# Performance work log

Measured on AMD Instinct MI355X. Metric: run time of the kernel, lower is better.

The kernel has to match this reference:

```python
import jax, jax.numpy as jnp
import numpy as np

N = 50000
E = 800000
DIM = 256
H = 8
HD = DIM // H


def setup_inputs() -> dict:
    key = jax.random.key(0)
    ks = jax.random.split(key, 8)
    s = 0.02
    return {
        "x": jax.random.normal(ks[0], (N, DIM), jnp.float32),
        "src": jax.random.randint(ks[1], (E,), 0, N, jnp.int32),
        "dst": jax.random.randint(ks[2], (E,), 0, N, jnp.int32),
        "Wqkv": jax.random.normal(ks[3], (DIM, 3 * DIM), jnp.float32) * s,
        "bqkv": jnp.zeros((3 * DIM,), jnp.float32),
        "Wout": jax.random.normal(ks[4], (DIM, DIM), jnp.float32) * s,
        "bout": jnp.zeros((DIM,), jnp.float32),
        "W1": jax.random.normal(ks[5], (2 * DIM, DIM), jnpp := jnp.float32) * s,
        "b1": jnp.zeros((DIM,), jnp.float32),
        "W2": jax.random.normal(ks[6], (DIM, DIM), jnp.float32) * s,
        "b2": jnp.zeros((DIM,), jnp.float32),
    }


def reference(x, src, dst, Wqkv, bqkv, Wout, bout, W1, b1, W2, b2):
    n = x.shape[0]
    scale = 1.0 / np.sqrt(HD).astype(np.float32)
    # QKV projection; torch reshapes [N, 3*dim] -> [N, H, 3*hd] then splits per head
    qkv = (x @ Wqkv + bqkv).reshape(n, H, 3 * HD)
    q, k, v = qkv[..., :HD], qkv[..., HD:2 * HD], qkv[..., 2 * HD:]
    # per-edge attention scores: key at src dotted with query at dst -> [E, H]
    scores = jnp.einsum('ehd,ehd->eh', k[src], q[dst]) * scale
    # edge softmax grouped by destination node
    m = jax.ops.segment_max(scores, dst, num_segments=n)  # [N, H]
    p = jnp.exp(scores - m[dst])
    denom = jax.ops.segment_sum(p, dst, num_segments=n)  # [N, H]
    probs = p / denom[dst]
    # weighted scatter-sum aggregation of source values -> [N, H, HD]
    agg = jax.ops.segment_sum(v[src] * probs[..., None], dst, num_segments=n)
    agg = agg.reshape(n, DIM) @ Wout + bout
    # feed-forward over concat([x, aggregated])
    h = jnp.concatenate([x, agg], axis=1)
    h = jax.nn.gelu(h @ W1 + b1, approximate=False)
    return h @ W2 + b2
```

## Files before the change

### kernel.cpp

```cpp
#include <hip/hip_runtime.h>
#include <hip/hip_bf16.h>
#include <math.h>

#define NDIM 256
#define HDIM 32
#define SCB 512

typedef __attribute__((ext_vector_type(8))) short bf16x8;
typedef __attribute__((ext_vector_type(4))) float f32x4;
typedef __attribute__((ext_vector_type(2))) float f32x2;
typedef unsigned long long ull;

__device__ inline float bf2f(unsigned short u) {
  union { unsigned int i; float f; } c; c.i = ((unsigned int)u) << 16; return c.f;
}
__device__ inline unsigned short f2bf(float f) {
  union { float f; unsigned int i; } c; c.f = f;
  unsigned int x = c.i;
  unsigned int lsb = (x >> 16) & 1u;
  x += 0x7fffu + lsb;
  return (unsigned short)(x >> 16);
}
__device__ inline float4 ldbf4(const unsigned short* p) {
  ull raw = *(const ull*)p;
  float4 f;
  f.x = bf2f((unsigned short)(raw));
  f.y = bf2f((unsigned short)(raw >> 16));
  f.z = bf2f((unsigned short)(raw >> 32));
  f.w = bf2f((unsigned short)(raw >> 48));
  return f;
}
__device__ inline void stbf4(unsigned short* p, float4 v) {
  ull raw = (ull)f2bf(v.x) | ((ull)f2bf(v.y) << 16)
          | ((ull)f2bf(v.z) << 32) | ((ull)f2bf(v.w) << 48);
  *(ull*)p = raw;
}
__device__ inline ull pk4_bf16(float v0, float v1, float v2, float v3) {
  return (ull)f2bf(v0) | ((ull)f2bf(v1) << 16) | ((ull)f2bf(v2) << 32) | ((ull)f2bf(v3) << 48);
}

__device__ inline unsigned char f2e4m3(float v) {
#if __has_builtin(__builtin_amdgcn_cvt_pk_fp8_f32)
  return (unsigned char)(__builtin_amdgcn_cvt_pk_fp8_f32(v, v, 0, false) & 0xff);
#else
  union { float f; unsigned int u; } c; c.f = v;
  unsigned char s = (unsigned char)((c.u >> 24) & 0x80);
  float a = fabsf(v);
  if (!(a < 448.f)) return (unsigned char)(s | 0x7e);
  if (a < 0.0009765625f) return s;
  int e = (int)((c.u >> 23) & 0xff) - 127;
  if (e < -6) {
    int q = (int)rintf(ldexpf(a, 9));
    if (q >= 8) return (unsigned char)(s | 0x08);
    return (unsigned char)(s | q);
  }
  int q = (int)rintf(ldexpf(a, 3 - e));
  if (q == 16) { e++; q = 8; }
  if (e > 8) return (unsigned char)(s | 0x7e);
  return (unsigned char)(s | ((e + 7) << 3) | (q - 8));
#endif
}
__device__ inline unsigned int pk4_e4m3(float v0, float v1, float v2, float v3) {
#if __has_builtin(__builtin_amdgcn_cvt_pk_fp8_f32)
  int w = __builtin_amdgcn_cvt_pk_fp8_f32(v0, v1, 0, false);
  w = __builtin_amdgcn_cvt_pk_fp8_f32(v2, v3, w, true);
  return (unsigned int)w;
#else
  return (unsigned int)f2e4m3(v0) | ((unsigned int)f2e4m3(v1) << 8)
       | ((unsigned int)f2e4m3(v2) << 16) | ((unsigned int)f2e4m3(v3) << 24);
#endif
}
template<bool HI>
__device__ inline f32x2 e4m3pk(unsigned int w) {
#if __has_builtin(__builtin_amdgcn_cvt_pk_f32_fp8)
  return __builtin_amdgcn_cvt_pk_f32_fp8((int)w, HI);
#else
  unsigned int h = HI ? (w >> 16) : w;
  f32x2 r;
  #pragma unroll
  for (int j = 0; j < 2; ++j) {
    unsigned char b = (unsigned char)(h >> (8 * j));
    int e = (b >> 3) & 0xf, mm = b & 7;
    float val = e ? ldexpf((float)(8 + mm), e - 10) : ldexpf((float)mm, -9);
    r[j] = (b & 0x80) ? -val : val;
  }
  return r;
#endif
}

__global__ void prep_k(
    const float* __restrict__ x, unsigned short* __restrict__ xb, int n8, int nbx,
    const float* __restrict__ Wqkv, unsigned short* __restrict__ wqkvt,
    const float* __restrict__ W1, unsigned short* __restrict__ wf,
    const float* __restrict__ W2, unsigned short* __restrict__ w2t,
    const float* __restrict__ Wout, const float* __restrict__ bout,
    const float* __restrict__ b1, float* __restrict__ bc)
{
  int b = blockIdx.x;
  int tid = threadIdx.x;
  if (b < nbx) {
    int i = b * 256 + tid;
    if (i < n8) {
      const float* p = x + (size_t)i * 8;
      float4 a = *(const float4*)p;
      float4 bv = *(const float4*)(p + 4);
      ull lo = (ull)f2bf(a.x) | ((ull)f2bf(a.y) << 16) | ((ull)f2bf(a.z) << 32) | ((ull)f2bf(a.w) << 48);
      ull hi = (ull)f2bf(bv.x) | ((ull)f2bf(bv.y) << 16) | ((ull)f2bf(bv.z) << 32) | ((ull)f2bf(bv.w) << 48);
      ull* d = (ull*)(xb + (size_t)i * 8);
      d[0] = lo; d[1] = hi;
    }
    return;
  }
  b -= nbx;
  int idx = b * 256 + tid;
  if (idx < 196608) {
    int j = idx >> 8, k = idx & 255;
    int seg = j >> 8, jj = j & 255;
    int h = jj >> 5, t = jj & 31;
    int orig = h * 96 + seg * 32 + t;
    wqkvt[(size_t)j * 256 + k] = f2bf(Wqkv[(size_t)k * 768 + orig]);
  } else if (idx < 262144) {
    int i2 = idx - 196608;
    int n = i2 >> 8, k = i2 & 255;
    wf[(size_t)n * 512 + k] = f2bf(W1[(size_t)k * 256 + n]);
  } else if (idx < 327680) {
    int i3 = idx - 262144;
    int n = i3 >> 8, k = i3 & 255;
    w2t[(size_t)n * 256 + k] = f2bf(W2[(size_t)k * 256 + n]);
  } else if (idx < 393216) {
    int i4 = idx - 327680;
    int a = i4 >> 8, n = i4 & 255;
    float s = 0.f;
    #pragma unroll 4
    for (int j = 0; j < 256; ++j)
      s += Wout[(size_t)a * 256 + j] * W1[(size_t)(256 + j) * 256 + n];
    wf[(size_t)n * 512 + 256 + a] = f2bf(s);
  } else if (idx < 393472) {
    int n = idx - 393216;
    float s = b1[n];
    for (int j = 0; j < 256; ++j)
      s += bout[j] * W1[(size_t)(256 + j) * 256 + n];
    bc[n] = s;
  }
}

__global__ __launch_bounds__(256, 4) void histqkv_k(
    const int* __restrict__ dstv, int* __restrict__ deg8,
    unsigned short* __restrict__ erank, int E, int Nn, int nhist,
    const unsigned short* __restrict__ A1, const unsigned short* __restrict__ Wt,
    const float* __restrict__ bias,
    unsigned short* __restrict__ Oq, unsigned char* __restrict__ Ok, unsigned char* __restrict__ Ov,
    int M)
{
  __shared__ char smem[32768];
  if (blockIdx.x < nhist) {
    int b = blockIdx.x;
    int e = b * 256 + threadIdx.x;
    if (e < E) {
      int rep = b & 7;
      int r = atomicAdd(&deg8[(size_t)rep * Nn + dstv[e]], 1);
      erank[e] = (unsigned short)r;
    }
    return;
  }
  unsigned short* As = (unsigned short*)smem;
  unsigned short* Bs = (unsigned short*)(smem + 16384);
  const int tid = threadIdx.x;
  const int lane = tid & 63;
  const int wid = tid >> 6;

  const int nwg = gridDim.x - nhist;
  const int bid = blockIdx.x - nhist;
  const int q8 = nwg >> 3, r8 = nwg & 7;
  const int xcd = bid & 7, idx8 = bid >> 3;
  const int swz = (xcd < r8 ? xcd * (q8 + 1) : r8 * (q8 + 1) + (xcd - r8) * q8) + idx8;
  const int nct = 6;
  const int bmt = swz / nct;
  const int bnt = swz - bmt * nct;
  const int bm = bmt * 128;
  const int bn = bnt * 128;

  const int wr = (wid >> 1) << 6;
  const int wc = (wid & 1) << 6;
  const int l15 = lane & 15, lhi = lane >> 4;
  const int srow = lane >> 3;
  const int ssl = (((lane & 7) ^ (lane >> 3)) << 3);

  f32x4 acc[4][4];
  #pragma unroll
  for (int i = 0; i < 4; ++i)
    #pragma unroll
    for (int j = 0; j < 4; ++j) acc[i][j] = (f32x4){0.f, 0.f, 0.f, 0.f};

  for (int k0 = 0; k0 < 256; k0 += 64) {
    #pragma unroll
    for (int t = 0; t < 4; ++t) {
      int qi = wid * 4 + t;
      const unsigned short* ga = A1 + (size_t)(bm + qi * 8 + srow) * 256 + k0 + ssl;
      __builtin_amdgcn_global_load_lds(
          (const __attribute__((address_space(1))) void*)ga,
          (__attribute__((address_space(3))) void*)&As[qi * 512], 16, 0, 0);
      const unsigned short* gb = Wt + (size_t)(bn + qi * 8 + srow) * 256 + k0 + ssl;
      __builtin_amdgcn_global_load_lds(
          (const __attribute__((address_space(1))) void*)gb,
          (__attribute__((address_space(3))) void*)&Bs[qi * 512], 16, 0, 0);
    }
    __syncthreads();
    #pragma unroll
    for (int kk = 0; kk < 64; kk += 32) {
      bf16x8 af[4], bfr[4];
      #pragma unroll
      for (int mi = 0; mi < 4; ++mi) {
        int rA = wr + mi * 16 + l15;
        af[mi] = *(const bf16x8*)&As[rA * 64 + ((((kk >> 3) + lhi) ^ (rA & 7)) << 3)];
      }
      #pragma unroll
      for (int ni = 0; ni < 4; ++ni) {
        int rB = wc + ni * 16 + l15;
        bfr[ni] = *(const bf16x8*)&Bs[rB * 64 + ((((kk >> 3) + lhi) ^ (rB & 7)) << 3)];
      }
      #pragma unroll
      for (int mi = 0; mi < 4; ++mi)
        #pragma unroll
        for (int ni = 0; ni < 4; ++ni)
          acc[mi][ni] = __builtin_amdgcn_mfma_f32_16x16x32_bf16(bfr[ni], af[mi], acc[mi][ni], 0, 0, 0);
    }
    __syncthreads();
  }

  const int seg = (bn + wc) >> 8;
  const int jjbase = (bn + wc) & 255;
  char* slabB = smem + wid * 8192;
  if (seg == 0) {
    #pragma unroll
    for (int ni = 0; ni < 4; ++ni) {
      int cl = ni * 16 + (lhi << 2);
      int jj = jjbase + cl;
      float4 bb = *(const float4*)&bias[(jj >> 5) * 96 + (jj & 31)];
      #pragma unroll
      for (int mi = 0; mi < 4; ++mi) {
        int rl = mi * 16 + l15;
        *(ull*)&slabB[rl * 128 + ((cl * 2) ^ ((rl & 7) << 4))] = pk4_bf16(
            acc[mi][ni][0] + bb.x, acc[mi][ni][1] + bb.y,
            acc[mi][ni][2] + bb.z, acc[mi][ni][3] + bb.w);
      }
    }
    asm volatile("s_waitcnt lgkmcnt(0)" ::: "memory");
    __builtin_amdgcn_sched_barrier(0);
    int rl0 = lane >> 3, co = (lane & 7) << 4;
    #pragma unroll
    for (int t = 0; t < 8; ++t) {
      int rl = t * 8 + rl0;
      int gr = bm + wr + rl;
      if (gr < M)
        *(float4*)&Oq[(size_t)gr * NDIM + jjbase + (co >> 1)] =
            *(float4*)&slabB[rl * 128 + (co ^ ((rl & 7) << 4))];
    }
  } else {
    unsigned char* dstp = (seg == 1) ? Ok : Ov;
    #pragma unroll
    for (int ni = 0; ni < 4; ++ni) {
      int cl = ni * 16 + (lhi << 2);
      int jj = jjbase + cl;
      float4 bb = *(const float4*)&bias[(jj >> 5) * 96 + seg * 32 + (jj & 31)];
      #pragma unroll
      for (int mi = 0; mi < 4; ++mi) {
        int rl = mi * 16 + l15;
        *(unsigned int*)&slabB[rl * 64 + (cl ^ ((rl & 3) << 4))] = pk4_e4m3(
            acc[mi][ni][0] + bb.x, acc[mi][ni][1] + bb.y,
            acc[mi][ni][2] + bb.z, acc[mi][ni][3] + bb.w);
      }
    }
    asm volatile("s_waitcnt lgkmcnt(0)" ::: "memory");
    __builtin_amdgcn_sched_barrier(0);
    int rl0 = lane >> 2, co = (lane & 3) << 4;
    #pragma unroll
    for (int t = 0; t < 4; ++t) {
      int rl = t * 16 + rl0;
      int gr = bm + wr + rl;
      if (gr < M)
        *(float4*)&dstp[(size_t)gr * NDIM + jjbase + co] =
            *(float4*)&slabB[rl * 64 + (co ^ ((rl & 3) << 4))];
    }
  }
}

__global__ __launch_bounds__(SCB) void bsum_k(const int* __restrict__ deg8, int* __restrict__ bsum, int n) {
  int tid = threadIdx.x;
  int i = blockIdx.x * SCB + tid;
  int v = 0;
  if (i < n) {
    #pragma unroll
    for (int r = 0; r < 8; ++r) v += deg8[(size_t)r * n + i];
  }
  #pragma unroll
  for (int d = 1; d < 64; d <<= 1) v += __shfl_xor(v, d);
  __shared__ int wsum[8];
  if ((tid & 63) == 0) wsum[tid >> 6] = v;
  __syncthreads();
  if (tid == 0) {
    int s = 0;
    #pragma unroll
    for (int j = 0; j < 8; ++j) s += wsum[j];
    bsum[blockIdx.x] = s;
  }
}

__global__ __launch_bounds__(128) void bscan_k(int* __restrict__ bsum, int nb) {
  __shared__ int tmp[128];
  int tid = threadIdx.x;
  int v = (tid < nb) ? bsum[tid] : 0;
  tmp[tid] = v;
  __syncthreads();
  for (int d = 1; d < 128; d <<= 1) {
    int t = (tid >= d) ? tmp[tid - d] : 0;
    __syncthreads();
    tmp[tid] += t;
    __syncthreads();
  }
  if (tid < nb) bsum[tid] = tmp[tid];
}

__global__ __launch_bounds__(SCB) void offs_k(const int* __restrict__ deg8, const int* __restrict__ bsum,
                                              int* __restrict__ offs, int* __restrict__ rbase, int n) {
  int tid = threadIdx.x, lane = tid & 63, wid = tid >> 6;
  int b = blockIdx.x;
  int i = b * SCB + tid;
  int c[8];
  int v = 0;
  if (i < n) {
    #pragma unroll
    for (int r = 0; r < 8; ++r) { c[r] = deg8[(size_t)r * n + i]; v += c[r]; }
  } else {
    #pragma unroll
    for (int r = 0; r < 8; ++r) c[r] = 0;
  }
  int incl = v;
  #pragma unroll
  for (int d = 1; d < 64; d <<= 1) { int t = __shfl_up(incl, d); if (lane >= d) incl += t; }
  __shared__ int wsum[8];
  if (lane == 63) wsum[wid] = incl;
  __syncthreads();
  if (tid < 8) {
    int s = wsum[tid];
    #pragma unroll
    for (int d = 1; d < 8; d <<= 1) { int t = __shfl_up(s, d); if (tid >= d) s += t; }
    wsum[tid] = s;
  }
  __syncthreads();
  int base = (b > 0 ? bsum[b - 1] : 0) + (wid > 0 ? wsum[wid - 1] : 0);
  if (i < n) {
    int start = base + incl - v;
    offs[i] = start;
    int p = start;
    #pragma unroll
    for (int r = 0; r < 8; ++r) { rbase[(size_t)r * n + i] = p; p += c[r]; }
  }
  if (i == n - 1) offs[n] = base + incl;
}

__global__ void scatter2_k(const int* __restrict__ src, const int* __restrict__ dstv,
                           const int* __restrict__ rbase, const unsigned short* __restrict__ erank,
                           int* __restrict__ ssrc, int E, int Nn) {
  int e = blockIdx.x * 256 + threadIdx.x;
  if (e < E) {
    int rep = (e >> 8) & 7;
    ssrc[rbase[(size_t)rep * Nn + dstv[e]] + erank[e]] = src[e];
  }
}

__global__ __launch_bounds__(256) void attn_k(
    const unsigned short* Q,
    const unsigned char* __restrict__ K8,
    const unsigned char* __restrict__ V8,
    const int* __restrict__ offs,
    const int* __restrict__ ssrc,
    unsigned short* agg, int N)
{
  int n = blockIdx.x * 4 + (threadIdx.x >> 6);
  if (n >= N) return;
  int lane = threadIdx.x & 63;
  int col = lane << 2;
  const float scale = 0.17677669529663689f;
  float4 q4 = ldbf4(Q + (size_t)n * NDIM + col);
  q4.x *= scale; q4.y *= scale; q4.z *= scale; q4.w *= scale;
  int e0 = offs[n], e1 = offs[n + 1];
  float den = 0.f;
  float ax = 0.f, ay = 0.f, az = 0.f, aw = 0.f;
  int e = e0;
  for (; e + 8 <= e1; e += 8) {
    unsigned int kw[8], vw[8];
    #pragma unroll
    for (int j = 0; j < 8; ++j) {
      int s = ssrc[e + j];
      kw[j] = *(const unsigned int*)(K8 + (size_t)s * NDIM + col);
      vw[j] = *(const unsigned int*)(V8 + (size_t)s * NDIM + col);
    }
    float d[8];
    #pragma unroll
    for (int j = 0; j < 8; ++j) {
      f32x2 k01 = e4m3pk<false>(kw[j]);
      f32x2 k23 = e4m3pk<true>(kw[j]);
      d[j] = q4.x * k01[0] + q4.y * k01[1] + q4.z * k23[0] + q4.w * k23[1];
    }
    #pragma unroll
    for (int j = 0; j < 8; ++j) {
      d[j] += __shfl_xor(d[j], 1);
      d[j] += __shfl_xor(d[j], 2);
      d[j] += __shfl_xor(d[j], 4);
    }
    #pragma unroll
    for (int j = 0; j < 8; ++j) {
      float p = __expf(d[j]);
      den += p;
      f32x2 v01 = e4m3pk<false>(vw[j]);
      f32x2 v23 = e4m3pk<true>(vw[j]);
      ax += p * v01[0]; ay += p * v01[1];
      az += p * v23[0]; aw += p * v23[1];
    }
  }
  for (; e + 4 <= e1; e += 4) {
    unsigned int kw[4], vw[4];
    #pragma unroll
    for (int j = 0; j < 4; ++j) {
      int s = ssrc[e + j];
      kw[j] = *(const unsigned int*)(K8 + (size_t)s * NDIM + col);
      vw[j] = *(const unsigned int*)(V8 + (size_t)s * NDIM + col);
    }
    float d[4];
    #pragma unroll
    for (int j = 0; j < 4; ++j) {
      f32x2 k01 = e4m3pk<false>(kw[j]);
      f32x2 k23 = e4m3pk<true>(kw[j]);
      d[j] = q4.x * k01[0] + q4.y * k01[1] + q4.z * k23[0] + q4.w * k23[1];
    }
    #pragma unroll
    for (int j = 0; j < 4; ++j) {
      d[j] += __shfl_xor(d[j], 1);
      d[j] += __shfl_xor(d[j], 2);
      d[j] += __shfl_xor(d[j], 4);
    }
    #pragma unroll
    for (int j = 0; j < 4; ++j) {
      float p = __expf(d[j]);
      den += p;
      f32x2 v01 = e4m3pk<false>(vw[j]);
      f32x2 v23 = e4m3pk<true>(vw[j]);
      ax += p * v01[0]; ay += p * v01[1];
      az += p * v23[0]; aw += p * v23[1];
    }
  }
  for (; e < e1; ++e) {
    int s = ssrc[e];
    unsigned int kw = *(const unsigned int*)(K8 + (size_t)s * NDIM + col);
    unsigned int vw = *(const unsigned int*)(V8 + (size_t)s * NDIM + col);
    f32x2 k01 = e4m3pk<false>(kw);
    f32x2 k23 = e4m3pk<true>(kw);
    float d = q4.x * k01[0] + q4.y * k01[1] + q4.z * k23[0] + q4.w * k23[1];
    d += __shfl_xor(d, 1);
    d += __shfl_xor(d, 2);
    d += __shfl_xor(d, 4);
    float p = __expf(d);
    den += p;
    f32x2 v01 = e4m3pk<false>(vw);
    f32x2 v23 = e4m3pk<true>(vw);
    ax += p * v01[0]; ay += p * v01[1];
    az += p * v23[0]; aw += p * v23[1];
  }
  float inv = (den > 0.f) ? 1.f / den : 0.f;
  stbf4(agg + (size_t)n * NDIM + col, make_float4(ax * inv, ay * inv, az * inv, aw * inv));
}

template<int EPI>
__global__ __launch_bounds__(256, 4) void mgemm_k(
    const unsigned short* __restrict__ A1, const unsigned short* __restrict__ A2,
    const unsigned short* __restrict__ Wt, const float* __restrict__ bias,
    float* __restrict__ Cf, unsigned short* __restrict__ Cb,
    int M, int K1, int K, int Ncol, int ldb, int nct)
{
  __shared__ char smem[32768];
  unsigned short* As = (unsigned short*)smem;
  unsigned short* Bs = (unsigned short*)(smem + 16384);
  const int tid = threadIdx.x;
  const int lane = tid & 63;
  const int wid = tid >> 6;

  const int nwg = gridDim.x;
  const int q8 = nwg >> 3, r8 = nwg & 7;
  const int xcd = blockIdx.x & 7, idx8 = blockIdx.x >> 3;
  const int swz = (xcd < r8 ? xcd * (q8 + 1) : r8 * (q8 + 1) + (xcd - r8) * q8) + idx8;
  const int bmt = swz / nct;
  const int bnt = swz - bmt * nct;
  const int bm = bmt * 128;
  const int bn = bnt * 128;

  const int wr = (wid >> 1) << 6;
  const int wc = (wid & 1) << 6;
  const int l15 = lane & 15, lhi = lane >> 4;
  const int srow = lane >> 3;
  const int ssl = (((lane & 7) ^ (lane >> 3)) << 3);

  f32x4 acc[4][4];
  #pragma unroll
  for (int i = 0; i < 4; ++i)
    #pragma unroll
    for (int j = 0; j < 4; ++j) acc[i][j] = (f32x4){0.f, 0.f, 0.f, 0.f};

  for (int k0 = 0; k0 < K; k0 += 64) {
    const unsigned short* Ab;
    int ks;
    if (k0 < K1) { Ab = A1; ks = k0; } else { Ab = A2; ks = k0 - K1; }
    #pragma unroll
    for (int t = 0; t < 4; ++t) {
      int qi = wid * 4 + t;
      const unsigned short* ga = Ab + (size_t)(bm + qi * 8 + srow) * 256 + ks + ssl;
      __builtin_amdgcn_global_load_lds(
          (const __attribute__((address_space(1))) void*)ga,
          (__attribute__((address_space(3))) void*)&As[qi * 512], 16, 0, 0);
      const unsigned short* gb = Wt + (size_t)(bn + qi * 8 + srow) * ldb + k0 + ssl;
      __builtin_amdgcn_global_load_lds(
          (const __attribute__((address_space(1))) void*)gb,
          (__attribute__((address_space(3))) void*)&Bs[qi * 512], 16, 0, 0);
    }
    __syncthreads();
    #pragma unroll
    for (int kk = 0; kk < 64; kk += 32) {
      bf16x8 af[4], bfr[4];
      #pragma unroll
      for (int mi = 0; mi < 4; ++mi) {
        int rA = wr + mi * 16 + l15;
        af[mi] = *(const bf16x8*)&As[rA * 64 + ((((kk >> 3) + lhi) ^ (rA & 7)) << 3)];
      }
      #pragma unroll
      for (int ni = 0; ni < 4; ++ni) {
        int rB = wc + ni * 16 + l15;
        bfr[ni] = *(const bf16x8*)&Bs[rB * 64 + ((((kk >> 3) + lhi) ^ (rB & 7)) << 3)];
      }
      #pragma unroll
      for (int mi = 0; mi < 4; ++mi)
        #pragma unroll
        for (int ni = 0; ni < 4; ++ni)
          acc[mi][ni] = __builtin_amdgcn_mfma_f32_16x16x32_bf16(bfr[ni], af[mi], acc[mi][ni], 0, 0, 0);
    }
    __syncthreads();
  }

  char* slabB = smem + wid * 8192;
  if (EPI == 0) {
    #pragma unroll
    for (int half = 0; half < 2; ++half) {
      #pragma unroll
      for (int nj = 0; nj < 2; ++nj) {
        int ni = half * 2 + nj;
        int cl = nj * 16 + (lhi << 2);
        float4 bb = *(const float4*)&bias[bn + wc + half * 32 + cl];
        #pragma unroll
        for (int mi = 0; mi < 4; ++mi) {
          int rl = mi * 16 + l15;
          *(float4*)&slabB[rl * 128 + ((cl * 4) ^ ((rl & 7) << 4))] = make_float4(
              acc[mi][ni][0] + bb.x, acc[mi][ni][1] + bb.y,
              acc[mi][ni][2] + bb.z, acc[mi][ni][3] + bb.w);
        }
      }
      asm volatile("s_waitcnt lgkmcnt(0)" ::: "memory");
      __builtin_amdgcn_sched_barrier(0);
      int rl0 = lane >> 3, co = (lane & 7) << 4;
      #pragma unroll
      for (int t = 0; t < 8; ++t) {
        int rl = t * 8 + rl0;
        int gr = bm + wr + rl;
        if (gr < M)
          *(float4*)&Cf[(size_t)gr * Ncol + bn + wc + half * 32 + (co >> 2)] =
              *(float4*)&slabB[rl * 128 + (co ^ ((rl & 7) << 4))];
      }
      if (half == 0) {
        asm volatile("s_waitcnt lgkmcnt(0)" ::: "memory");
        __builtin_amdgcn_sched_barrier(0);
      }
    }
  } else {
    #pragma unroll
    for (int ni = 0; ni < 4; ++ni) {
      int cl = ni * 16 + (lhi << 2);
      float4 bb = *(const float4*)&bias[bn + wc + cl];
      #pragma unroll
      for (int mi = 0; mi < 4; ++mi) {
        int rl = mi * 16 + l15;
        float v0 = acc[mi][ni][0] + bb.x;
        float v1 = acc[mi][ni][1] + bb.y;
        float v2 = acc[mi][ni][2] + bb.z;
        float v3 = acc[mi][ni][3] + bb.w;
        v0 = 0.5f * v0 * (1.0f + erff(v0 * 0.70710678118654752f));
        v1 = 0.5f * v1 * (1.0f + erff(v1 * 0.70710678118654752f));
        v2 = 0.5f * v2 * (1.0f + erff(v2 * 0.70710678118654752f));
        v3 = 0.5f * v3 * (1.0f + erff(v3 * 0.70710678118654752f));
        *(ull*)&slabB[rl * 128 + ((cl * 2) ^ ((rl & 7) << 4))] = pk4_bf16(v0, v1, v2, v3);
      }
    }
    asm volatile("s_waitcnt lgkmcnt(0)" ::: "memory");
    __builtin_amdgcn_sched_barrier(0);
    int rl0 = lane >> 3, co = (lane & 7) << 4;
    #pragma unroll
    for (int t = 0; t < 8; ++t) {
      int rl = t * 8 + rl0;
      int gr = bm + wr + rl;
      if (gr < M)
        *(float4*)&Cb[(size_t)gr * Ncol + bn + wc + (co >> 1)] =
            *(float4*)&slabB[rl * 128 + (co ^ ((rl & 7) << 4))];
    }
  }
}

extern "C" void kernel_launch(void* const* d_in, const int* in_sizes, int n_in,
                              void* d_out, int out_size, void* d_ws, size_t ws_size,
                              hipStream_t stream) {
  (void)n_in; (void)out_size; (void)ws_size;
  const float* x    = (const float*)d_in[0];
  const int*   src  = (const int*)d_in[1];
  const int*   dst  = (const int*)d_in[2];
  const float* Wqkv = (const float*)d_in[3];
  const float* bqkv = (const float*)d_in[4];
  const float* Wout = (const float*)d_in[5];
  const float* bout = (const float*)d_in[6];
  const float* W1   = (const float*)d_in[7];
  const float* b1   = (const float*)d_in[8];
  const float* W2   = (const float*)d_in[9];
  const float* b2   = (const float*)d_in[10];
  float* out = (float*)d_out;

  const int N = in_sizes[0] / NDIM;
  const int E = in_sizes[1];
  const int Mp = (N + 127) & ~127;
  const int nb = (N + SCB - 1) / SCB;

  char* ws = (char*)d_ws;
  size_t off = 0;
  auto alloc = [&](size_t bytes) -> char* {
    char* p = ws + off;
    off += (bytes + 255) & ~(size_t)255;
    return p;
  };
  unsigned short* xb   = (unsigned short*)alloc((size_t)Mp * NDIM * 2);
  unsigned short* Q    = (unsigned short*)alloc((size_t)Mp * NDIM * 2);
  unsigned short* Kb   = (unsigned short*)alloc((size_t)Mp * NDIM * 2);
  unsigned short* Vb   = (unsigned short*)alloc((size_t)Mp * NDIM * 2);
  unsigned short* wqkvt = (unsigned short*)alloc((size_t)768 * 256 * 2);
  unsigned short* wft   = (unsigned short*)alloc((size_t)256 * 512 * 2);
  unsigned short* w2t   = (unsigned short*)alloc((size_t)256 * 256 * 2);
  float*          bc    = (float*)alloc(256 * 4);
  int* deg8   = (int*)alloc((size_t)8 * N * 4);
  int* rbase  = (int*)alloc((size_t)8 * N * 4);
  int* offs   = (int*)alloc((size_t)(N + 1) * 4);
  unsigned short* erank = (unsigned short*)alloc((size_t)E * 2);
  int* ssrc   = (int*)alloc((size_t)E * 4);
  int* bsum   = (int*)alloc((size_t)nb * 4);

  unsigned char* K8 = (unsigned char*)Kb;
  unsigned char* V8 = (unsigned char*)Vb;
  unsigned short* agg = Q;
  unsigned short* h1  = Kb;

  const int n8  = N * NDIM / 8;
  const int nbx = (n8 + 255) / 256;
  const int nbw = (393472 + 255) / 256;
  const int nsc = (E + 255) / 256;
  const int mt  = Mp / 128;

  hipMemsetAsync(deg8, 0, (size_t)8 * N * 4, stream);

  prep_k<<<nbx + nbw, 256, 0, stream>>>(
      x, xb, n8, nbx, Wqkv, wqkvt, W1, wft, W2, w2t, Wout, bout, b1, bc);

  histqkv_k<<<nsc + mt * 6, 256, 0, stream>>>(
      dst, deg8, erank, E, N, nsc,
      xb, wqkvt, bqkv, Q, K8, V8, N);

  bsum_k<<<nb, SCB, 0, stream>>>(deg8, bsum, N);
  bscan_k<<<1, 128, 0, stream>>>(bsum, nb);
  offs_k<<<nb, SCB, 0, stream>>>(deg8, bsum, offs, rbase, N);

  scatter2_k<<<nsc, 256, 0, stream>>>(src, dst, rbase, erank, ssrc, E, N);

  attn_k<<<(N + 3) / 4, 256, 0, stream>>>(Q, K8, V8, offs, ssrc, agg, N);

  mgemm_k<2><<<mt * 2, 256, 0, stream>>>(
      xb, agg, wft, bc, nullptr, h1, N, 256, 512, 256, 512, 2);

  mgemm_k<0><<<mt * 2, 256, 0, stream>>>(
      h1, nullptr, w2t, b2, out, nullptr, N, 256, 256, 256, 256, 2);
}
```

Before: 221.2 us.

## Fuse FFN W1+GELU and W2 GEMMs into one kernel keeping hidden in LDS

Replaces the two separate FFN GEMM launches with one kernel. Each block owns 64 rows and all 256 output columns, computes the W1 GEMM plus GELU into a swizzled bf16 tile in shared memory, then runs the W2 GEMM reading that tile and W2 straight from global memory. This removes the global round trip of the hidden activation and one launch. In exchange it uses 72KB of shared memory with fewer blocks per CU, loads the full W1 slice per block, and reads W2 fragments without LDS staging.

```diff
diff --git a/kernel.cpp b/kernel.cpp
--- a/kernel.cpp
+++ b/kernel.cpp
@@ -471,31 +471,22 @@
   stbf4(agg + (size_t)n * NDIM + col, make_float4(ax * inv, ay * inv, az * inv, aw * inv));
 }
 
-template<int EPI>
-__global__ __launch_bounds__(256, 4) void mgemm_k(
-    const unsigned short* __restrict__ A1, const unsigned short* __restrict__ A2,
-    const unsigned short* __restrict__ Wt, const float* __restrict__ bias,
-    float* __restrict__ Cf, unsigned short* __restrict__ Cb,
-    int M, int K1, int K, int Ncol, int ldb, int nct)
+__global__ __launch_bounds__(256, 2) void ffnw2_k(
+    const unsigned short* __restrict__ xb, const unsigned short* __restrict__ agg,
+    const unsigned short* __restrict__ wft, const float* __restrict__ bc,
+    const unsigned short* __restrict__ w2t, const float* __restrict__ b2,
+    float* __restrict__ out, int M)
 {
-  __shared__ char smem[32768];
-  unsigned short* As = (unsigned short*)smem;
-  unsigned short* Bs = (unsigned short*)(smem + 16384);
+  __shared__ char smem[73728];
+  unsigned short* As1 = (unsigned short*)smem;
+  unsigned short* Bs1 = (unsigned short*)(smem + 8192);
+  unsigned short* hS  = (unsigned short*)(smem + 40960);
+
   const int tid = threadIdx.x;
   const int lane = tid & 63;
   const int wid = tid >> 6;
-
-  const int nwg = gridDim.x;
-  const int q8 = nwg >> 3, r8 = nwg & 7;
-  const int xcd = blockIdx.x & 7, idx8 = blockIdx.x >> 3;
-  const int swz = (xcd < r8 ? xcd * (q8 + 1) : r8 * (q8 + 1) + (xcd - r8) * q8) + idx8;
-  const int bmt = swz / nct;
-  const int bnt = swz - bmt * nct;
-  const int bm = bmt * 128;
-  const int bn = bnt * 128;
-
-  const int wr = (wid >> 1) << 6;
-  const int wc = (wid & 1) << 6;
+  const int bm = blockIdx.x * 64;
+  const int wc = wid << 6;
   const int l15 = lane & 15, lhi = lane >> 4;
   const int srow = lane >> 3;
   const int ssl = (((lane & 7) ^ (lane >> 3)) << 3);
@@ -506,21 +497,24 @@
     #pragma unroll
     for (int j = 0; j < 4; ++j) acc[i][j] = (f32x4){0.f, 0.f, 0.f, 0.f};
 
-  for (int k0 = 0; k0 < K; k0 += 64) {
-    const unsigned short* Ab;
-    int ks;
-    if (k0 < K1) { Ab = A1; ks = k0; } else { Ab = A2; ks = k0 - K1; }
-    #pragma unroll
-    for (int t = 0; t < 4; ++t) {
-      int qi = wid * 4 + t;
+  for (int k0 = 0; k0 < 512; k0 += 64) {
+    const unsigned short* Ab = (k0 < 256) ? xb : agg;
+    int ks = k0 & 255;
+    #pragma unroll
+    for (int t = 0; t < 2; ++t) {
+      int qi = wid * 2 + t;
       const unsigned short* ga = Ab + (size_t)(bm + qi * 8 + srow) * 256 + ks + ssl;
       __builtin_amdgcn_global_load_lds(
           (const __attribute__((address_space(1))) void*)ga,
-          (__attribute__((address_space(3))) void*)&As[qi * 512], 16, 0, 0);
-      const unsigned short* gb = Wt + (size_t)(bn + qi * 8 + srow) * ldb + k0 + ssl;
+          (__attribute__((address_space(3))) void*)&As1[qi * 512], 16, 0, 0);
+    }
+    #pragma unroll
+    for (int t = 0; t < 8; ++t) {
+      int qi = wid * 8 + t;
+      const unsigned short* gb = wft + (size_t)(qi * 8 + srow) * 512 + k0 + ssl;
       __builtin_amdgcn_global_load_lds(
           (const __attribute__((address_space(1))) void*)gb,
-          (__attribute__((address_space(3))) void*)&Bs[qi * 512], 16, 0, 0);
+          (__attribute__((address_space(3))) void*)&Bs1[qi * 512], 16, 0, 0);
     }
     __syncthreads();
     #pragma unroll
@@ -528,13 +522,13 @@
       bf16x8 af[4], bfr[4];
       #pragma unroll
       for (int mi = 0; mi < 4; ++mi) {
-        int rA = wr + mi * 16 + l15;
-        af[mi] = *(const bf16x8*)&As[rA * 64 + ((((kk >> 3) + lhi) ^ (rA & 7)) << 3)];
+        int rA = mi * 16 + l15;
+        af[mi] = *(const bf16x8*)&As1[rA * 64 + ((((kk >> 3) + lhi) ^ (rA & 7)) << 3)];
       }
       #pragma unroll
       for (int ni = 0; ni < 4; ++ni) {
         int rB = wc + ni * 16 + l15;
-        bfr[ni] = *(const bf16x8*)&Bs[rB * 64 + ((((kk >> 3) + lhi) ^ (rB & 7)) << 3)];
+        bfr[ni] = *(const bf16x8*)&Bs1[rB * 64 + ((((kk >> 3) + lhi) ^ (rB & 7)) << 3)];
       }
       #pragma unroll
       for (int mi = 0; mi < 4; ++mi)
@@ -545,56 +539,68 @@
     __syncthreads();
   }
 
+  #pragma unroll
+  for (int ni = 0; ni < 4; ++ni) {
+    int c0 = wc + ni * 16 + (lhi << 2);
+    float4 bb = *(const float4*)&bc[c0];
+    #pragma unroll
+    for (int mi = 0; mi < 4; ++mi) {
+      int r = mi * 16 + l15;
+      float v0 = acc[mi][ni][0] + bb.x;
+      float v1 = acc[mi][ni][1] + bb.y;
+      float v2 = acc[mi][ni][2] + bb.z;
+      float v3 = acc[mi][ni][3] + bb.w;
+      v0 = 0.5f * v0 * (1.0f + erff(v0 * 0.70710678118654752f));
+      v1 = 0.5f * v1 * (1.0f + erff(v1 * 0.70710678118654752f));
+      v2 = 0.5f * v2 * (1.0f + erff(v2 * 0.70710678118654752f));
+      v3 = 0.5f * v3 * (1.0f + erff(v3 * 0.70710678118654752f));
+      *(ull*)((char*)hS + r * 512 + ((c0 * 2) ^ ((r & 7) << 4))) = pk4_bf16(v0, v1, v2, v3);
+    }
+  }
+  __syncthreads();
+
+  f32x4 acc2[4][4];
+  #pragma unroll
+  for (int i = 0; i < 4; ++i)
+    #pragma unroll
+    for (int j = 0; j < 4; ++j) acc2[i][j] = (f32x4){0.f, 0.f, 0.f, 0.f};
+
+  for (int c = 0; c < 4; ++c) {
+    #pragma unroll
+    for (int kk = 0; kk < 64; kk += 32) {
+      bf16x8 af[4], bfr[4];
+      #pragma unroll
+      for (int mi = 0; mi < 4; ++mi) {
+        int r = mi * 16 + l15;
+        int kidx = c * 64 + kk + lhi * 8;
+        af[mi] = *(const bf16x8*)((char*)hS + r * 512 + ((kidx * 2) ^ ((r & 7) << 4)));
+      }
+      #pragma unroll
+      for (int ni = 0; ni < 4; ++ni) {
+        bfr[ni] = *(const bf16x8*)&w2t[(size_t)(wc + ni * 16 + l15) * 256 + c * 64 + kk + lhi * 8];
+      }
+      #pragma unroll
+      for (int mi = 0; mi < 4; ++mi)
+        #pragma unroll
+        for (int ni = 0; ni < 4; ++ni)
+          acc2[mi][ni] = __builtin_amdgcn_mfma_f32_16x16x32_bf16(bfr[ni], af[mi], acc2[mi][ni], 0, 0, 0);
+    }
+  }
+
   char* slabB = smem + wid * 8192;
-  if (EPI == 0) {
-    #pragma unroll
-    for (int half = 0; half < 2; ++half) {
-      #pragma unroll
-      for (int nj = 0; nj < 2; ++nj) {
-        int ni = half * 2 + nj;
-        int cl = nj * 16 + (lhi << 2);
-        float4 bb = *(const float4*)&bias[bn + wc + half * 32 + cl];
-        #pragma unroll
-        for (int mi = 0; mi < 4; ++mi) {
-          int rl = mi * 16 + l15;
-          *(float4*)&slabB[rl * 128 + ((cl * 4) ^ ((rl & 7) << 4))] = make_float4(
-              acc[mi][ni][0] + bb.x, acc[mi][ni][1] + bb.y,
-              acc[mi][ni][2] + bb.z, acc[mi][ni][3] + bb.w);
-        }
-      }
-      asm volatile("s_waitcnt lgkmcnt(0)" ::: "memory");
-      __builtin_amdgcn_sched_barrier(0);
-      int rl0 = lane >> 3, co = (lane & 7) << 4;
-      #pragma unroll
-      for (int t = 0; t < 8; ++t) {
-        int rl = t * 8 + rl0;
-        int gr = bm + wr + rl;
-        if (gr < M)
-          *(float4*)&Cf[(size_t)gr * Ncol + bn + wc + half * 32 + (co >> 2)] =
-              *(float4*)&slabB[rl * 128 + (co ^ ((rl & 7) << 4))];
-      }
-      if (half == 0) {
-        asm volatile("s_waitcnt lgkmcnt(0)" ::: "memory");
-        __builtin_amdgcn_sched_barrier(0);
-      }
-    }
-  } else {
-    #pragma unroll
-    for (int ni = 0; ni < 4; ++ni) {
-      int cl = ni * 16 + (lhi << 2);
-      float4 bb = *(const float4*)&bias[bn + wc + cl];
+  #pragma unroll
+  for (int half = 0; half < 2; ++half) {
+    #pragma unroll
+    for (int nj = 0; nj < 2; ++nj) {
+      int ni = half * 2 + nj;
+      int cl = nj * 16 + (lhi << 2);
+      float4 bb = *(const float4*)&b2[wc + half * 32 + cl];
       #pragma unroll
       for (int mi = 0; mi < 4; ++mi) {
         int rl = mi * 16 + l15;
-        float v0 = acc[mi][ni][0] + bb.x;
-        float v1 = acc[mi][ni][1] + bb.y;
-        float v2 = acc[mi][ni][2] + bb.z;
-        float v3 = acc[mi][ni][3] + bb.w;
-        v0 = 0.5f * v0 * (1.0f + erff(v0 * 0.70710678118654752f));
-        v1 = 0.5f * v1 * (1.0f + erff(v1 * 0.70710678118654752f));
-        v2 = 0.5f * v2 * (1.0f + erff(v2 * 0.70710678118654752f));
-        v3 = 0.5f * v3 * (1.0f + erff(v3 * 0.70710678118654752f));
-        *(ull*)&slabB[rl * 128 + ((cl * 2) ^ ((rl & 7) << 4))] = pk4_bf16(v0, v1, v2, v3);
+        *(float4*)&slabB[rl * 128 + ((cl * 4) ^ ((rl & 7) << 4))] = make_float4(
+            acc2[mi][ni][0] + bb.x, acc2[mi][ni][1] + bb.y,
+            acc2[mi][ni][2] + bb.z, acc2[mi][ni][3] + bb.w);
       }
     }
     asm volatile("s_waitcnt lgkmcnt(0)" ::: "memory");
@@ -603,10 +609,14 @@
     #pragma unroll
     for (int t = 0; t < 8; ++t) {
       int rl = t * 8 + rl0;
-      int gr = bm + wr + rl;
+      int gr = bm + rl;
       if (gr < M)
-        *(float4*)&Cb[(size_t)gr * Ncol + bn + wc + (co >> 1)] =
+        *(float4*)&out[(size_t)gr * 256 + wc + half * 32 + (co >> 2)] =
             *(float4*)&slabB[rl * 128 + (co ^ ((rl & 7) << 4))];
+    }
+    if (half == 0) {
+      asm volatile("s_waitcnt lgkmcnt(0)" ::: "memory");
+      __builtin_amdgcn_sched_barrier(0);
     }
   }
 }
@@ -658,7 +668,6 @@
   unsigned char* K8 = (unsigned char*)Kb;
   unsigned char* V8 = (unsigned char*)Vb;
   unsigned short* agg = Q;
-  unsigned short* h1  = Kb;
 
   const int n8  = N * NDIM / 8;
   const int nbx = (n8 + 255) / 256;
@@ -683,9 +692,6 @@
 
   attn_k<<<(N + 3) / 4, 256, 0, stream>>>(Q, K8, V8, offs, ssrc, agg, N);
 
-  mgemm_k<2><<<mt * 2, 256, 0, stream>>>(
-      xb, agg, wft, bc, nullptr, h1, N, 256, 512, 256, 512, 2);
-
-  mgemm_k<0><<<mt * 2, 256, 0, stream>>>(
-      h1, nullptr, w2t, b2, out, nullptr, N, 256, 256, 256, 256, 2);
-}
+  ffnw2_k<<<Mp / 64, 256, 0, stream>>>(
+      xb, agg, wft, bc, w2t, b2, out, N);
+}
```

New measurement: 230.4 us. 4.1% more time.

## Precompute x-half of FFN1 GEMM in QKV kernel and enlarge attention blocks

Applied to the files above, without the earlier changes.

Adds extra workgroups to the combined histogram/QKV kernel that compute x @ W1[:256] + bias into a bf16 partial buffer. The later FFN1 GEMM then runs only over the aggregated half (K=256) and adds the partial before GELU. This moves half of that GEMM off the critical path after attention, where it can overlap with the histogram and QKV work, at the cost of an extra N×256 bf16 buffer write and read. The attention kernel also now uses 512-thread blocks covering 8 nodes instead of 4.

```diff
diff --git a/kernel.cpp b/kernel.cpp
--- a/kernel.cpp
+++ b/kernel.cpp
@@ -3,7 +3,6 @@
 #include <math.h>
 
 #define NDIM 256
-#define HDIM 32
 #define SCB 512
 
 typedef __attribute__((ext_vector_type(8))) short bf16x8;
@@ -146,11 +145,12 @@
 
 __global__ __launch_bounds__(256, 4) void histqkv_k(
     const int* __restrict__ dstv, int* __restrict__ deg8,
-    unsigned short* __restrict__ erank, int E, int Nn, int nhist,
+    unsigned short* __restrict__ erank, int E, int Nn, int nhist, int nqkv,
     const unsigned short* __restrict__ A1, const unsigned short* __restrict__ Wt,
     const float* __restrict__ bias,
     unsigned short* __restrict__ Oq, unsigned char* __restrict__ Ok, unsigned char* __restrict__ Ov,
-    int M)
+    const unsigned short* __restrict__ wft, const float* __restrict__ bcp,
+    unsigned short* __restrict__ Pb, int M)
 {
   __shared__ char smem[32768];
   if (blockIdx.x < nhist) {
@@ -168,23 +168,12 @@
   const int tid = threadIdx.x;
   const int lane = tid & 63;
   const int wid = tid >> 6;
-
-  const int nwg = gridDim.x - nhist;
-  const int bid = blockIdx.x - nhist;
-  const int q8 = nwg >> 3, r8 = nwg & 7;
-  const int xcd = bid & 7, idx8 = bid >> 3;
-  const int swz = (xcd < r8 ? xcd * (q8 + 1) : r8 * (q8 + 1) + (xcd - r8) * q8) + idx8;
-  const int nct = 6;
-  const int bmt = swz / nct;
-  const int bnt = swz - bmt * nct;
-  const int bm = bmt * 128;
-  const int bn = bnt * 128;
-
   const int wr = (wid >> 1) << 6;
   const int wc = (wid & 1) << 6;
   const int l15 = lane & 15, lhi = lane >> 4;
   const int srow = lane >> 3;
   const int ssl = (((lane & 7) ^ (lane >> 3)) << 3);
+  const int bid = blockIdx.x - nhist;
 
   f32x4 acc[4][4];
   #pragma unroll
@@ -192,51 +181,158 @@
     #pragma unroll
     for (int j = 0; j < 4; ++j) acc[i][j] = (f32x4){0.f, 0.f, 0.f, 0.f};
 
-  for (int k0 = 0; k0 < 256; k0 += 64) {
-    #pragma unroll
-    for (int t = 0; t < 4; ++t) {
-      int qi = wid * 4 + t;
-      const unsigned short* ga = A1 + (size_t)(bm + qi * 8 + srow) * 256 + k0 + ssl;
-      __builtin_amdgcn_global_load_lds(
-          (const __attribute__((address_space(1))) void*)ga,
-          (__attribute__((address_space(3))) void*)&As[qi * 512], 16, 0, 0);
-      const unsigned short* gb = Wt + (size_t)(bn + qi * 8 + srow) * 256 + k0 + ssl;
-      __builtin_amdgcn_global_load_lds(
-          (const __attribute__((address_space(1))) void*)gb,
-          (__attribute__((address_space(3))) void*)&Bs[qi * 512], 16, 0, 0);
-    }
-    __syncthreads();
-    #pragma unroll
-    for (int kk = 0; kk < 64; kk += 32) {
-      bf16x8 af[4], bfr[4];
-      #pragma unroll
-      for (int mi = 0; mi < 4; ++mi) {
-        int rA = wr + mi * 16 + l15;
-        af[mi] = *(const bf16x8*)&As[rA * 64 + ((((kk >> 3) + lhi) ^ (rA & 7)) << 3)];
-      }
+  if (bid < nqkv) {
+    const int q8 = nqkv >> 3, r8 = nqkv & 7;
+    const int xcd = bid & 7, idx8 = bid >> 3;
+    const int swz = (xcd < r8 ? xcd * (q8 + 1) : r8 * (q8 + 1) + (xcd - r8) * q8) + idx8;
+    const int bmt = swz / 6;
+    const int bnt = swz - bmt * 6;
+    const int bm = bmt * 128;
+    const int bn = bnt * 128;
+
+    for (int k0 = 0; k0 < 256; k0 += 64) {
+      #pragma unroll
+      for (int t = 0; t < 4; ++t) {
+        int qi = wid * 4 + t;
+        const unsigned short* ga = A1 + (size_t)(bm + qi * 8 + srow) * 256 + k0 + ssl;
+        __builtin_amdgcn_global_load_lds(
+            (const __attribute__((address_space(1))) void*)ga,
+            (__attribute__((address_space(3))) void*)&As[qi * 512], 16, 0, 0);
+        const unsigned short* gb = Wt + (size_t)(bn + qi * 8 + srow) * 256 + k0 + ssl;
+        __builtin_amdgcn_global_load_lds(
+            (const __attribute__((address_space(1))) void*)gb,
+            (__attribute__((address_space(3))) void*)&Bs[qi * 512], 16, 0, 0);
+      }
+      __syncthreads();
+      #pragma unroll
+      for (int kk = 0; kk < 64; kk += 32) {
+        bf16x8 af[4], bfr[4];
+        #pragma unroll
+        for (int mi = 0; mi < 4; ++mi) {
+          int rA = wr + mi * 16 + l15;
+          af[mi] = *(const bf16x8*)&As[rA * 64 + ((((kk >> 3) + lhi) ^ (rA & 7)) << 3)];
+        }
+        #pragma unroll
+        for (int ni = 0; ni < 4; ++ni) {
+          int rB = wc + ni * 16 + l15;
+          bfr[ni] = *(const bf16x8*)&Bs[rB * 64 + ((((kk >> 3) + lhi) ^ (rB & 7)) << 3)];
+        }
+        #pragma unroll
+        for (int mi = 0; mi < 4; ++mi)
+          #pragma unroll
+          for (int ni = 0; ni < 4; ++ni)
+            acc[mi][ni] = __builtin_amdgcn_mfma_f32_16x16x32_bf16(bfr[ni], af[mi], acc[mi][ni], 0, 0, 0);
+      }
+      __syncthreads();
+    }
+
+    const int seg = (bn + wc) >> 8;
+    const int jjbase = (bn + wc) & 255;
+    char* slabB = smem + wid * 8192;
+    if (seg == 0) {
       #pragma unroll
       for (int ni = 0; ni < 4; ++ni) {
-        int rB = wc + ni * 16 + l15;
-        bfr[ni] = *(const bf16x8*)&Bs[rB * 64 + ((((kk >> 3) + lhi) ^ (rB & 7)) << 3)];
-      }
-      #pragma unroll
-      for (int mi = 0; mi < 4; ++mi)
-        #pragma unroll
-        for (int ni = 0; ni < 4; ++ni)
-          acc[mi][ni] = __builtin_amdgcn_mfma_f32_16x16x32_bf16(bfr[ni], af[mi], acc[mi][ni], 0, 0, 0);
-    }
-    __syncthreads();
-  }
-
-  const int seg = (bn + wc) >> 8;
-  const int jjbase = (bn + wc) & 255;
-  char* slabB = smem + wid * 8192;
-  if (seg == 0) {
+        int cl = ni * 16 + (lhi << 2);
+        int jj = jjbase + cl;
+        float4 bb = *(const float4*)&bias[(jj >> 5) * 96 + (jj & 31)];
+        #pragma unroll
+        for (int mi = 0; mi < 4; ++mi) {
+          int rl = mi * 16 + l15;
+          *(ull*)&slabB[rl * 128 + ((cl * 2) ^ ((rl & 7) << 4))] = pk4_bf16(
+              acc[mi][ni][0] + bb.x, acc[mi][ni][1] + bb.y,
+              acc[mi][ni][2] + bb.z, acc[mi][ni][3] + bb.w);
+        }
+      }
+      asm volatile("s_waitcnt lgkmcnt(0)" ::: "memory");
+      __builtin_amdgcn_sched_barrier(0);
+      int rl0 = lane >> 3, co = (lane & 7) << 4;
+      #pragma unroll
+      for (int t = 0; t < 8; ++t) {
+        int rl = t * 8 + rl0;
+        int gr = bm + wr + rl;
+        if (gr < M)
+          *(float4*)&Oq[(size_t)gr * NDIM + jjbase + (co >> 1)] =
+              *(float4*)&slabB[rl * 128 + (co ^ ((rl & 7) << 4))];
+      }
+    } else {
+      unsigned char* dstp = (seg == 1) ? Ok : Ov;
+      #pragma unroll
+      for (int ni = 0; ni < 4; ++ni) {
+        int cl = ni * 16 + (lhi << 2);
+        int jj = jjbase + cl;
+        float4 bb = *(const float4*)&bias[(jj >> 5) * 96 + seg * 32 + (jj & 31)];
+        #pragma unroll
+        for (int mi = 0; mi < 4; ++mi) {
+          int rl = mi * 16 + l15;
+          *(unsigned int*)&slabB[rl * 64 + (cl ^ ((rl & 3) << 4))] = pk4_e4m3(
+              acc[mi][ni][0] + bb.x, acc[mi][ni][1] + bb.y,
+              acc[mi][ni][2] + bb.z, acc[mi][ni][3] + bb.w);
+        }
+      }
+      asm volatile("s_waitcnt lgkmcnt(0)" ::: "memory");
+      __builtin_amdgcn_sched_barrier(0);
+      int rl0 = lane >> 2, co = (lane & 3) << 4;
+      #pragma unroll
+      for (int t = 0; t < 4; ++t) {
+        int rl = t * 16 + rl0;
+        int gr = bm + wr + rl;
+        if (gr < M)
+          *(float4*)&dstp[(size_t)gr * NDIM + jjbase + co] =
+              *(float4*)&slabB[rl * 64 + (co ^ ((rl & 3) << 4))];
+      }
+    }
+  } else {
+    const int nP = gridDim.x - nhist - nqkv;
+    const int pid = bid - nqkv;
+    const int q8 = nP >> 3, r8 = nP & 7;
+    const int xcd = pid & 7, idx8 = pid >> 3;
+    const int swz = (xcd < r8 ? xcd * (q8 + 1) : r8 * (q8 + 1) + (xcd - r8) * q8) + idx8;
+    const int bmt = swz >> 1;
+    const int bnt = swz & 1;
+    const int bm = bmt * 128;
+    const int bn = bnt * 128;
+
+    for (int k0 = 0; k0 < 256; k0 += 64) {
+      #pragma unroll
+      for (int t = 0; t < 4; ++t) {
+        int qi = wid * 4 + t;
+        const unsigned short* ga = A1 + (size_t)(bm + qi * 8 + srow) * 256 + k0 + ssl;
+        __builtin_amdgcn_global_load_lds(
+            (const __attribute__((address_space(1))) void*)ga,
+            (__attribute__((address_space(3))) void*)&As[qi * 512], 16, 0, 0);
+        const unsigned short* gb = wft + (size_t)(bn + qi * 8 + srow) * 512 + k0 + ssl;
+        __builtin_amdgcn_global_load_lds(
+            (const __attribute__((address_space(1))) void*)gb,
+            (__attribute__((address_space(3))) void*)&Bs[qi * 512], 16, 0, 0);
+      }
+      __syncthreads();
+      #pragma unroll
+      for (int kk = 0; kk < 64; kk += 32) {
+        bf16x8 af[4], bfr[4];
+        #pragma unroll
+        for (int mi = 0; mi < 4; ++mi) {
+          int rA = wr + mi * 16 + l15;
+          af[mi] = *(const bf16x8*)&As[rA * 64 + ((((kk >> 3) + lhi) ^ (rA & 7)) << 3)];
+        }
+        #pragma unroll
+        for (int ni = 0; ni < 4; ++ni) {
+          int rB = wc + ni * 16 + l15;
+          bfr[ni] = *(const bf16x8*)&Bs[rB * 64 + ((((kk >> 3) + lhi) ^ (rB & 7)) << 3)];
+        }
+        #pragma unroll
+        for (int mi = 0; mi < 4; ++mi)
+          #pragma unroll
+          for (int ni = 0; ni < 4; ++ni)
+            acc[mi][ni] = __builtin_amdgcn_mfma_f32_16x16x32_bf16(bfr[ni], af[mi], acc[mi][ni], 0, 0, 0);
+      }
+      __syncthreads();
+    }
+
+    char* slabB = smem + wid * 8192;
     #pragma unroll
     for (int ni = 0; ni < 4; ++ni) {
       int cl = ni * 16 + (lhi << 2);
-      int jj = jjbase + cl;
-      float4 bb = *(const float4*)&bias[(jj >> 5) * 96 + (jj & 31)];
+      float4 bb = *(const float4*)&bcp[bn + wc + cl];
       #pragma unroll
       for (int mi = 0; mi < 4; ++mi) {
         int rl = mi * 16 + l15;
@@ -252,35 +348,8 @@
     for (int t = 0; t < 8; ++t) {
       int rl = t * 8 + rl0;
       int gr = bm + wr + rl;
-      if (gr < M)
-        *(float4*)&Oq[(size_t)gr * NDIM + jjbase + (co >> 1)] =
-            *(float4*)&slabB[rl * 128 + (co ^ ((rl & 7) << 4))];
-    }
-  } else {
-    unsigned char* dstp = (seg == 1) ? Ok : Ov;
-    #pragma unroll
-    for (int ni = 0; ni < 4; ++ni) {
-      int cl = ni * 16 + (lhi << 2);
-      int jj = jjbase + cl;
-      float4 bb = *(const float4*)&bias[(jj >> 5) * 96 + seg * 32 + (jj & 31)];
-      #pragma unroll
-      for (int mi = 0; mi < 4; ++mi) {
-        int rl = mi * 16 + l15;
-        *(unsigned int*)&slabB[rl * 64 + (cl ^ ((rl & 3) << 4))] = pk4_e4m3(
-            acc[mi][ni][0] + bb.x, acc[mi][ni][1] + bb.y,
-            acc[mi][ni][2] + bb.z, acc[mi][ni][3] + bb.w);
-      }
-    }
-    asm volatile("s_waitcnt lgkmcnt(0)" ::: "memory");
-    __builtin_amdgcn_sched_barrier(0);
-    int rl0 = lane >> 2, co = (lane & 3) << 4;
-    #pragma unroll
-    for (int t = 0; t < 4; ++t) {
-      int rl = t * 16 + rl0;
-      int gr = bm + wr + rl;
-      if (gr < M)
-        *(float4*)&dstp[(size_t)gr * NDIM + jjbase + co] =
-            *(float4*)&slabB[rl * 64 + (co ^ ((rl & 3) << 4))];
+      *(float4*)&Pb[(size_t)gr * 256 + bn + wc + (co >> 1)] =
+          *(float4*)&slabB[rl * 128 + (co ^ ((rl & 7) << 4))];
     }
   }
 }
@@ -369,7 +438,7 @@
   }
 }
 
-__global__ __launch_bounds__(256) void attn_k(
+__global__ __launch_bounds__(512) void attn_k(
     const unsigned short* Q,
     const unsigned char* __restrict__ K8,
     const unsigned char* __restrict__ V8,
@@ -377,7 +446,7 @@
     const int* __restrict__ ssrc,
     unsigned short* agg, int N)
 {
-  int n = blockIdx.x * 4 + (threadIdx.x >> 6);
+  int n = blockIdx.x * 8 + (threadIdx.x >> 6);
   if (n >= N) return;
   int lane = threadIdx.x & 63;
   int col = lane << 2;
@@ -475,6 +544,7 @@
 __global__ __launch_bounds__(256, 4) void mgemm_k(
     const unsigned short* __restrict__ A1, const unsigned short* __restrict__ A2,
     const unsigned short* __restrict__ Wt, const float* __restrict__ bias,
+    const unsigned short* __restrict__ Pb,
     float* __restrict__ Cf, unsigned short* __restrict__ Cb,
     int M, int K1, int K, int Ncol, int ldb, int nct)
 {
@@ -582,14 +652,26 @@
     #pragma unroll
     for (int ni = 0; ni < 4; ++ni) {
       int cl = ni * 16 + (lhi << 2);
-      float4 bb = *(const float4*)&bias[bn + wc + cl];
+      float4 bb;
+      if (EPI == 2) bb = *(const float4*)&bias[bn + wc + cl];
       #pragma unroll
       for (int mi = 0; mi < 4; ++mi) {
         int rl = mi * 16 + l15;
-        float v0 = acc[mi][ni][0] + bb.x;
-        float v1 = acc[mi][ni][1] + bb.y;
-        float v2 = acc[mi][ni][2] + bb.z;
-        float v3 = acc[mi][ni][3] + bb.w;
+        int gr = bm + wr + rl;
+        float v0, v1, v2, v3;
+        if (EPI == 2) {
+          v0 = acc[mi][ni][0] + bb.x;
+          v1 = acc[mi][ni][1] + bb.y;
+          v2 = acc[mi][ni][2] + bb.z;
+          v3 = acc[mi][ni][3] + bb.w;
+        } else {
+          float4 pv = (gr < M) ? ldbf4(&Pb[(size_t)gr * 256 + bn + wc + cl])
+                               : make_float4(0.f, 0.f, 0.f, 0.f);
+          v0 = acc[mi][ni][0] + pv.x;
+          v1 = acc[mi][ni][1] + pv.y;
+          v2 = acc[mi][ni][2] + pv.z;
+          v3 = acc[mi][ni][3] + pv.w;
+        }
         v0 = 0.5f * v0 * (1.0f + erff(v0 * 0.70710678118654752f));
         v1 = 0.5f * v1 * (1.0f + erff(v1 * 0.70710678118654752f));
         v2 = 0.5f * v2 * (1.0f + erff(v2 * 0.70710678118654752f));
@@ -614,7 +696,7 @@
 extern "C" void kernel_launch(void* const* d_in, const int* in_sizes, int n_in,
                               void* d_out, int out_size, void* d_ws, size_t ws_size,
                               hipStream_t stream) {
-  (void)n_in; (void)out_size; (void)ws_size;
+  (void)n_in; (void)out_size;
   const float* x    = (const float*)d_in[0];
   const int*   src  = (const int*)d_in[1];
   const int*   dst  = (const int*)d_in[2];
@@ -654,6 +736,10 @@
   unsigned short* erank = (unsigned short*)alloc((size_t)E * 2);
   int* ssrc   = (int*)alloc((size_t)E * 4);
   int* bsum   = (int*)alloc((size_t)nb * 4);
+  size_t off_noP = off;
+  unsigned short* Pb = (unsigned short*)alloc((size_t)Mp * 256 * 2);
+  const bool useP = (off <= ws_size);
+  (void)off_noP;
 
   unsigned char* K8 = (unsigned char*)Kb;
   unsigned char* V8 = (unsigned char*)Vb;
@@ -665,15 +751,17 @@
   const int nbw = (393472 + 255) / 256;
   const int nsc = (E + 255) / 256;
   const int mt  = Mp / 128;
+  const int nqkv = mt * 6;
+  const int nP = useP ? mt * 2 : 0;
 
   hipMemsetAsync(deg8, 0, (size_t)8 * N * 4, stream);
 
   prep_k<<<nbx + nbw, 256, 0, stream>>>(
       x, xb, n8, nbx, Wqkv, wqkvt, W1, wft, W2, w2t, Wout, bout, b1, bc);
 
-  histqkv_k<<<nsc + mt * 6, 256, 0, stream>>>(
-      dst, deg8, erank, E, N, nsc,
-      xb, wqkvt, bqkv, Q, K8, V8, N);
+  histqkv_k<<<nsc + nqkv + nP, 256, 0, stream>>>(
+      dst, deg8, erank, E, N, nsc, nqkv,
+      xb, wqkvt, bqkv, Q, K8, V8, wft, bc, Pb, N);
 
   bsum_k<<<nb, SCB, 0, stream>>>(deg8, bsum, N);
   bscan_k<<<1, 128, 0, stream>>>(bsum, nb);
@@ -681,11 +769,16 @@
 
   scatter2_k<<<nsc, 256, 0, stream>>>(src, dst, rbase, erank, ssrc, E, N);
 
-  attn_k<<<(N + 3) / 4, 256, 0, stream>>>(Q, K8, V8, offs, ssrc, agg, N);
-
-  mgemm_k<2><<<mt * 2, 256, 0, stream>>>(
-      xb, agg, wft, bc, nullptr, h1, N, 256, 512, 256, 512, 2);
+  attn_k<<<(N + 7) / 8, 512, 0, stream>>>(Q, K8, V8, offs, ssrc, agg, N);
+
+  if (useP) {
+    mgemm_k<3><<<mt * 2, 256, 0, stream>>>(
+        agg, nullptr, wft + 256, bc, Pb, nullptr, h1, N, 256, 256, 256, 512, 2);
+  } else {
+    mgemm_k<2><<<mt * 2, 256, 0, stream>>>(
+        xb, agg, wft, bc, nullptr, nullptr, h1, N, 256, 512, 256, 512, 2);
+  }
 
   mgemm_k<0><<<mt * 2, 256, 0, stream>>>(
-      h1, nullptr, w2t, b2, out, nullptr, N, 256, 256, 256, 256, 2);
-}
+      h1, nullptr, w2t, b2, nullptr, out, nullptr, N, 256, 256, 256, 256, 2);
+}
```

New measurement: 238.4 us. +7.8%, slower.
